# Optimization experiments

Hardware: AMD Instinct MI355X
Metric: run time of the kernel (lower is better)

Reference implementation:

```python
import jax, jax.numpy as jnp
import numpy as np

LAYERS = 2
HEADS = 4
TYPE_IDX = 1  # type='logic' -> 1
HIDDEN = 256
HEAD_DIM = HIDDEN // HEADS
EPS = 1e-6


def setup_inputs() -> dict:
    key = jax.random.key(0)
    ks = jax.random.split(key, 12)
    B, S, H = 4, 2048, HIDDEN
    inputs = jax.random.normal(ks[0], (B, S, H), jnp.float32)
    graphs = jax.random.uniform(ks[1], (B, 2, S, S), jnp.float32)
    biases_batch = jax.random.normal(ks[2], (B, 2, S, S), jnp.float32)
    s_h = 1.0 / np.sqrt(H).astype(np.float32)
    s_d = 1.0 / np.sqrt(HEAD_DIM).astype(np.float32)
    gc_w = jax.random.normal(ks[3], (LAYERS, H, H), jnp.float32) * s_h
    gc_b = jnp.zeros((LAYERS, H), jnp.float32)
    attn_w = jax.random.normal(ks[4], (LAYERS, HEAD_DIM, H), jnp.float32) * s_h  # conv1 (1x1) weight
    attn_a = jax.random.normal(ks[5], (LAYERS, HEAD_DIM), jnp.float32) * s_d     # conv2_1 (1x1) weight
    ln_a = jnp.ones((H,), jnp.float32)
    ln_b = jnp.zeros((H,), jnp.float32)
    w1 = jax.random.normal(ks[6], (H, H), jnp.float32) * s_h
    w1b = jnp.zeros((H,), jnp.float32)
    w2 = jax.random.normal(ks[7], (H, H), jnp.float32) * s_h
    w2b = jnp.zeros((H,), jnp.float32)
    return dict(inputs=inputs, graphs=graphs, biases_batch=biases_batch,
                gc_w=gc_w, gc_b=gc_b, attn_w=attn_w, attn_a=attn_a,
                ln_a=ln_a, ln_b=ln_b, w1=w1, w1b=w1b, w2=w2, w2b=w2b)


def reference(inputs, graphs, biases_batch, gc_w, gc_b, attn_w, attn_a, ln_a, ln_b, w1, w1b, w2, w2b):
    adj = graphs[:, TYPE_IDX]          # [b,s,s]
    bias = biases_batch[:, TYPE_IDX]   # [b,s,s]
    x0 = inputs
    x = inputs
    for i in range(LAYERS):
        # GraphConvolution: adj @ (x @ W) + b
        mf = jnp.einsum('bij,bjh->bih', adj, x @ gc_w[i]) + gc_b[i]
        # Node_Attn_head (NOTE: original uses conv2_1 for BOTH f_1 and f_2)
        seq_fts = jnp.einsum('bsh,dh->bsd', mf, attn_w[i])      # [b,s,d]
        f = seq_fts @ attn_a[i]                                  # [b,s]
        logits = jax.nn.leaky_relu(f[:, :, None] + f[:, None, :])  # f_2^T + f_1 -> [b,s,s]
        coefs = jax.nn.softmax(logits + bias, axis=1)            # Softmax(dim=1)
        ret = jax.nn.leaky_relu(jnp.einsum('bij,bjd->bid', coefs, seq_fts))  # [b,s,d]
        # shared attention head across all HEADS -> identical outputs, concatenated
        x = jnp.tile(ret, (1, 1, HEADS)) + x
    # LayerNorm (torch.std is unbiased -> ddof=1), residual to original inputs
    mean = x.mean(-1, keepdims=True)
    std = jnp.std(x, axis=-1, keepdims=True, ddof=1)
    g = ln_a * (x - mean) / (std + EPS) + ln_b + x0
    # PositionwiseFeedForward (dropout inactive in eval)
    ff = jax.nn.relu(g @ w1.T + w1b) @ w2.T + w2b
    return ff + g
```

## Files before the change

### kernel.cpp

```cpp
#include <hip/hip_runtime.h>
#include <math.h>

#define BB 4
#define SS 2048
#define HH 256
#define DD 64
#define NLAYERS 2
#define NPART 128

#define XSC  (1.f/64.f)
#define XSCI 64.f
#define FSC  (1.f/256.f)
#define WSC  256.f
#define LNWSC 5.5451774444795624f

typedef _Float16 f16;
typedef f16 half8 __attribute__((ext_vector_type(8)));
typedef f16 half4 __attribute__((ext_vector_type(4)));
typedef float f32x4 __attribute__((ext_vector_type(4)));
#define MFMA16(a, b, c) __builtin_amdgcn_mfma_f32_16x16x32_f16(a, b, c, 0, 0, 0)

__device__ __forceinline__ float lrelu(float v) { return v > 0.f ? v : 0.01f * v; }
__device__ __forceinline__ int enc(float f) { int i = __float_as_int(f); return i >= 0 ? i : (i ^ 0x7fffffff); }
__device__ __forceinline__ float dec(int k) { int i = k >= 0 ? k : (k ^ 0x7fffffff); return __int_as_float(i); }
__device__ __forceinline__ void split8(const float* v, half8& h, half8& l) {
    #pragma unroll
    for (int e = 0; e < 8; ++e) {
        f16 hh = (f16)v[e]; h[e] = hh; l[e] = (f16)((v[e] - (float)hh) * 2048.f);
    }
}

__global__ __launch_bounds__(256) void split_scale(
    const float* __restrict__ src, f16* __restrict__ dh, f16* __restrict__ dl, float scale)
{
    long i = ((long)blockIdx.x * 256 + threadIdx.x) * 8;
    float4 a = *(const float4*)&src[i];
    float4 b = *(const float4*)&src[i + 4];
    float v[8] = {a.x * scale, a.y * scale, a.z * scale, a.w * scale,
                  b.x * scale, b.y * scale, b.z * scale, b.w * scale};
    half8 h, l; split8(v, h, l);
    *(half8*)&dh[i] = h; *(half8*)&dl[i] = l;
}

__global__ __launch_bounds__(256) void prep_wy(
    const float* __restrict__ gc_w, const float* __restrict__ gc_b,
    const float* __restrict__ attn_w,
    f16* __restrict__ WysH, f16* __restrict__ WysL, float* __restrict__ by,
    const float* __restrict__ w1, const float* __restrict__ w2,
    f16* __restrict__ w1h, f16* __restrict__ w1l,
    f16* __restrict__ w2h, f16* __restrict__ w2l, int* __restrict__ FMXi)
{
    int L = blockIdx.x >> 6, d = blockIdx.x & 63;
    int h = threadIdx.x;
    const float* gwr = gc_w + (long)L * HH * HH + (long)h * HH;
    const float* aw = attn_w + (long)L * DD * HH + (long)d * HH;
    float acc = 0.f;
    #pragma unroll 4
    for (int hp = 0; hp < HH; hp += 4) {
        float4 g4 = *(const float4*)&gwr[hp];
        float4 a4 = *(const float4*)&aw[hp];
        acc += g4.x * a4.x + g4.y * a4.y + g4.z * a4.z + g4.w * a4.w;
    }
    f16 hh = (f16)acc;
    WysH[((long)L * DD + d) * HH + h] = hh;
    WysL[((long)L * DD + d) * HH + h] = (f16)((acc - (float)hh) * 2048.f);
    if (h == 0) {
        float ba = 0.f;
        const float* gb = gc_b + (long)L * HH;
        for (int hp = 0; hp < HH; ++hp) ba += gb[hp] * aw[hp];
        by[L * DD + d] = ba;
    }
    int gt = blockIdx.x * 256 + h;
    #pragma unroll
    for (int p = 0; p < 4; ++p) {
        int e = gt * 4 + p;
        if (e < 65536) {
            float v = w1[e]; f16 x = (f16)v;
            w1h[e] = x; w1l[e] = (f16)((v - (float)x) * 2048.f);
        } else {
            int e2 = e - 65536;
            float v = w2[e2]; f16 x = (f16)v;
            w2h[e2] = x; w2l[e2] = (f16)((v - (float)x) * 2048.f);
        }
    }
    if (blockIdx.x == 0 && h < 2 * BB) FMXi[h] = enc(-1e30f);
}

__global__ __launch_bounds__(256) void y_mfma(
    const f16* __restrict__ xh, const f16* __restrict__ xl,
    const f16* __restrict__ WyhL, const f16* __restrict__ WylL,
    f16* __restrict__ yTh, f16* __restrict__ yTl)
{
    const int tid = threadIdx.x;
    const int w = tid >> 6, l = tid & 63;
    const int gw = blockIdx.x * 4 + w;
    const int b = gw >> 7, st = gw & 127;
    const int s0 = st * 16;
    const int lr = l & 15, kg = (l >> 4) * 8;
    const f16* Aph = xh + ((long)b * SS + s0 + lr) * HH;
    const f16* Apl = xl + ((long)b * SS + s0 + lr) * HH;
    f32x4 acch[4] = {}, accm[4] = {};
    #pragma unroll
    for (int k0 = 0; k0 < HH; k0 += 32) {
        half8 ah = *(const half8*)(Aph + k0 + kg);
        half8 al = *(const half8*)(Apl + k0 + kg);
        #pragma unroll
        for (int dt = 0; dt < 4; ++dt) {
            long boff = (long)(dt * 16 + lr) * HH + k0 + kg;
            half8 bh = *(const half8*)(WyhL + boff);
            half8 bl = *(const half8*)(WylL + boff);
            acch[dt] = MFMA16(ah, bh, acch[dt]);
            accm[dt] = MFMA16(ah, bl, accm[dt]);
            accm[dt] = MFMA16(al, bh, accm[dt]);
        }
    }
    const int rg0 = (l >> 4) * 4;
    #pragma unroll
    for (int dt = 0; dt < 4; ++dt) {
        int d = dt * 16 + lr;
        half4 h4, l4;
        #pragma unroll
        for (int rr = 0; rr < 4; ++rr) {
            float v = acch[dt][rr] + accm[dt][rr] * (1.f / 2048.f);
            f16 hh = (f16)v; h4[rr] = hh; l4[rr] = (f16)((v - (float)hh) * 2048.f);
        }
        long ob = ((long)b * DD + d) * SS + s0 + rg0;
        *(half4*)(yTh + ob) = h4;
        *(half4*)(yTl + ob) = l4;
    }
}

__global__ __launch_bounds__(512, 2) void ftp_fused(
    const float* __restrict__ adjB,
    const f16* __restrict__ yTh, const f16* __restrict__ yTl,
    const float* __restrict__ byL, const float* __restrict__ aaL,
    float* __restrict__ F, f16* __restrict__ fTh, f16* __restrict__ fTl,
    int* __restrict__ fmxSlot)
{
    __shared__ float Ls[8][16][68];
    __shared__ float fmaxS[16];
    const int b = blockIdx.y;
    const int i0 = blockIdx.x * 16;
    const int tid = threadIdx.x;
    const int w = tid >> 6, l = tid & 63, lr = l & 15, kg = (l >> 4) * 8;
    const float* Arow = adjB + (long)b * 2 * SS * SS + (long)(i0 + lr) * SS;
    const f16* Bh = yTh + ((long)b * DD + lr) * SS;
    const f16* Bl = yTl + ((long)b * DD + lr) * SS;

    f32x4 acch[4] = {}, accm[4] = {};
    #pragma unroll
    for (int ks = 0; ks < 256; ks += 32) {
        int k = w * 256 + ks + kg;
        float4 a0 = *(const float4*)(Arow + k);
        float4 a1 = *(const float4*)(Arow + k + 4);
        float av[8] = {a0.x, a0.y, a0.z, a0.w, a1.x, a1.y, a1.z, a1.w};
        half8 ah, al; split8(av, ah, al);
        #pragma unroll
        for (int dt = 0; dt < 4; ++dt) {
            long off = (long)dt * 16 * SS + k;
            half8 bh = *(const half8*)(Bh + off);
            half8 bl = *(const half8*)(Bl + off);
            acch[dt] = MFMA16(ah, bh, acch[dt]);
            accm[dt] = MFMA16(ah, bl, accm[dt]);
            accm[dt] = MFMA16(al, bh, accm[dt]);
        }
    }
    const int rg0 = (l >> 4) * 4;
    #pragma unroll
    for (int dt = 0; dt < 4; ++dt)
        #pragma unroll
        for (int rr = 0; rr < 4; ++rr)
            Ls[w][rg0 + rr][dt * 16 + lr] = acch[dt][rr] + accm[dt][rr] * (1.f / 2048.f);
    __syncthreads();

    {
        int r = tid >> 5, q = tid & 31, c0 = q * 2;
        float s0 = 0.f, s1 = 0.f;
        #pragma unroll
        for (int ww = 0; ww < 8; ++ww) { s0 += Ls[ww][r][c0]; s1 += Ls[ww][r][c0 + 1]; }
        s0 = s0 * XSCI + byL[c0];
        s1 = s1 * XSCI + byL[c0 + 1];
        Ls[0][r][c0] = s0; Ls[0][r][c0 + 1] = s1;
        float dot = s0 * aaL[c0] + s1 * aaL[c0 + 1];
        dot += __shfl_xor(dot, 1, 64);
        dot += __shfl_xor(dot, 2, 64);
        dot += __shfl_xor(dot, 4, 64);
        dot += __shfl_xor(dot, 8, 64);
        dot += __shfl_xor(dot, 16, 64);
        if (q == 0) { F[b * SS + i0 + r] = dot; fmaxS[r] = dot; }
    }
    __syncthreads();
    if (tid == 0) {
        float m = -1e30f;
        #pragma unroll
        for (int r = 0; r < 16; ++r) m = fmaxf(m, fmaxS[r]);
        atomicMax(fmxSlot + b, enc(m));
    }
    if (tid < 256) {
        int d = tid >> 2, sq = (tid & 3) * 4;
        half4 h4, l4;
        #pragma unroll
        for (int e = 0; e < 4; ++e) {
            float v = Ls[0][sq + e][d] * FSC;
            f16 hh = (f16)v; h4[e] = hh; l4[e] = (f16)((v - (float)hh) * 2048.f);
        }
        long ob = ((long)b * DD + d) * SS + i0 + sq;
        *(half4*)(fTh + ob) = h4;
        *(half4*)(fTl + ob) = l4;
    }
}

__global__ __launch_bounds__(512) void col_stats_part(
    const float* __restrict__ biasb, const float* __restrict__ f,
    const int* __restrict__ fmxSlot,
    float* __restrict__ partS, float* __restrict__ Mv)
{
    __shared__ float fs[32];
    const int b = blockIdx.z;
    const int chunk = blockIdx.y;
    const int half = threadIdx.x >> 8;
    const int t = threadIdx.x & 255;
    const int j0 = blockIdx.x * 1024 + t * 4;
    const float* bb = biasb + (long)b * 2 * SS * SS;
    const int ibase = chunk * 32 + half * 16;

    if (threadIdx.x < 32) fs[threadIdx.x] = f[b * SS + chunk * 32 + threadIdx.x];

    float fj[4], M[4], s[4] = {0.f, 0.f, 0.f, 0.f};
    const float fmx = dec(fmxSlot[b]);
    #pragma unroll
    for (int q = 0; q < 4; ++q) {
        fj[q] = f[b * SS + j0 + q];
        M[q] = lrelu(fmx + fj[q]) + 8.f;
    }
    __syncthreads();

    #pragma unroll
    for (int ii = 0; ii < 16; ii += 2) {
        float fi0 = fs[half * 16 + ii], fi1 = fs[half * 16 + ii + 1];
        float4 b0 = *(const float4*)&bb[(long)(ibase + ii) * SS + j0];
        float4 b1 = *(const float4*)&bb[(long)(ibase + ii + 1) * SS + j0];
        s[0] += __expf(lrelu(fi0 + fj[0]) + b0.x - M[0]);
        s[1] += __expf(lrelu(fi0 + fj[1]) + b0.y - M[1]);
        s[2] += __expf(lrelu(fi0 + fj[2]) + b0.z - M[2]);
        s[3] += __expf(lrelu(fi0 + fj[3]) + b0.w - M[3]);
        s[0] += __expf(lrelu(fi1 + fj[0]) + b1.x - M[0]);
        s[1] += __expf(lrelu(fi1 + fj[1]) + b1.y - M[1]);
        s[2] += __expf(lrelu(fi1 + fj[2]) + b1.z - M[2]);
        s[3] += __expf(lrelu(fi1 + fj[3]) + b1.w - M[3]);
    }
    const int c = chunk * 2 + half;
    #pragma unroll
    for (int q = 0; q < 4; ++q)
        partS[((long)c * BB + b) * SS + j0 + q] = s[q];
    if (chunk == 0 && half == 0) {
        #pragma unroll
        for (int q = 0; q < 4; ++q) Mv[b * SS + j0 + q] = M[q];
    }
}

__global__ __launch_bounds__(256) void col_stats_merge(
    const float* __restrict__ partS, const float* __restrict__ Mv,
    float* __restrict__ Cv)
{
    __shared__ float red[4][64];
    const int b = blockIdx.y;
    const int jl = threadIdx.x & 63;
    const int p = threadIdx.x >> 6;
    const int j = blockIdx.x * 64 + jl;
    float s = 0.f;
    #pragma unroll
    for (int k = 0; k < 32; ++k)
        s += partS[((long)(p * 32 + k) * BB + b) * SS + j];
    red[p][jl] = s;
    __syncthreads();
    if (p == 0) {
        float tot = ((red[0][jl] + red[1][jl]) + (red[2][jl] + red[3][jl]));
        Cv[b * SS + j] = LNWSC - __logf(tot) - Mv[b * SS + j];
    }
}

__global__ __launch_bounds__(512, 2) void pvp_fused(
    const float* __restrict__ biasb, const float* __restrict__ f,
    const float* __restrict__ Cv,
    const f16* __restrict__ fTh, const f16* __restrict__ fTl,
    const float* __restrict__ xin, float* __restrict__ X,
    f16* __restrict__ xh, f16* __restrict__ xl, int writeSplit)
{
    __shared__ float Ls[8][16][68];
    const int b = blockIdx.y;
    const int i0 = blockIdx.x * 16;
    const int tid = threadIdx.x;
    const int w = tid >> 6, l = tid & 63, lr = l & 15, kg = (l >> 4) * 8;
    const int irow = i0 + lr;
    const float fi = f[b * SS + irow];
    const float* brow = biasb + (long)b * 2 * SS * SS + (long)irow * SS;
    const float* fb = f + b * SS;
    const float* cb = Cv + b * SS;
    const f16* Bh = fTh + ((long)b * DD + lr) * SS;
    const f16* Bl = fTl + ((long)b * DD + lr) * SS;

    f32x4 acch[4] = {}, accm[4] = {};
    #pragma unroll
    for (int jc = 0; jc < 256; jc += 32) {
        const int jb = w * 256 + jc + kg;
        float4 bs0 = *(const float4*)(brow + jb);
        float4 bs1 = *(const float4*)(brow + jb + 4);
        float4 fj0 = *(const float4*)(fb + jb);
        float4 fj1 = *(const float4*)(fb + jb + 4);
        float4 cj0 = *(const float4*)(cb + jb);
        float4 cj1 = *(const float4*)(cb + jb + 4);
        float wv[8];
        wv[0] = __expf(lrelu(fi + fj0.x) + bs0.x + cj0.x);
        wv[1] = __expf(lrelu(fi + fj0.y) + bs0.y + cj0.y);
        wv[2] = __expf(lrelu(fi + fj0.z) + bs0.z + cj0.z);
        wv[3] = __expf(lrelu(fi + fj0.w) + bs0.w + cj0.w);
        wv[4] = __expf(lrelu(fi + fj1.x) + bs1.x + cj1.x);
        wv[5] = __expf(lrelu(fi + fj1.y) + bs1.y + cj1.y);
        wv[6] = __expf(lrelu(fi + fj1.z) + bs1.z + cj1.z);
        wv[7] = __expf(lrelu(fi + fj1.w) + bs1.w + cj1.w);
        half8 ah, al; split8(wv, ah, al);
        #pragma unroll
        for (int dt = 0; dt < 4; ++dt) {
            long off = (long)dt * 16 * SS + jb;
            half8 bh = *(const half8*)(Bh + off);
            half8 bl = *(const half8*)(Bl + off);
            acch[dt] = MFMA16(ah, bh, acch[dt]);
            accm[dt] = MFMA16(ah, bl, accm[dt]);
            accm[dt] = MFMA16(al, bh, accm[dt]);
        }
    }
    const int rg0 = (l >> 4) * 4;
    #pragma unroll
    for (int dt = 0; dt < 4; ++dt)
        #pragma unroll
        for (int rr = 0; rr < 4; ++rr)
            Ls[w][rg0 + rr][dt * 16 + lr] = acch[dt][rr] + accm[dt][rr] * (1.f / 2048.f);
    __syncthreads();

    {
        int r = tid >> 5, q = tid & 31, dq = q * 2;
        float v0 = 0.f, v1 = 0.f;
        #pragma unroll
        for (int ww = 0; ww < 8; ++ww) { v0 += Ls[ww][r][dq]; v1 += Ls[ww][r][dq + 1]; }
        v0 = lrelu(v0); v1 = lrelu(v1);
        long rowoff = ((long)b * SS + i0 + r) * HH;
        #pragma unroll
        for (int rep = 0; rep < 4; ++rep) {
            long off = rowoff + rep * DD + dq;
            float o0 = v0 + xin[off];
            float o1 = v1 + xin[off + 1];
            X[off] = o0; X[off + 1] = o1;
            if (writeSplit) {
                float s0 = o0 * XSC, s1 = o1 * XSC;
                f16 h0 = (f16)s0, h1 = (f16)s1;
                xh[off] = h0; xl[off] = (f16)((s0 - (float)h0) * 2048.f);
                xh[off + 1] = h1; xl[off + 1] = (f16)((s1 - (float)h1) * 2048.f);
            }
        }
    }
}

__global__ __launch_bounds__(256) void layernorm_g(
    const float* __restrict__ x, const float* __restrict__ x0,
    const float* __restrict__ lna, const float* __restrict__ lnb,
    float* __restrict__ g, f16* __restrict__ gh, f16* __restrict__ gl)
{
    const int wave = threadIdx.x >> 6, lane = threadIdx.x & 63;
    const long row = (long)blockIdx.x * 4 + wave;
    const int c0 = lane * 4;
    float4 v = *(const float4*)&x[row * HH + c0];
    float s = v.x + v.y + v.z + v.w;
    #pragma unroll
    for (int off = 32; off; off >>= 1) s += __shfl_xor(s, off, 64);
    float mean = s * (1.f / HH);
    float dx = v.x - mean, dy = v.y - mean, dz = v.z - mean, dw = v.w - mean;
    float sq = dx * dx + dy * dy + dz * dz + dw * dw;
    #pragma unroll
    for (int off = 32; off; off >>= 1) sq += __shfl_xor(sq, off, 64);
    float stdv = sqrtf(sq * (1.f / (HH - 1)));
    float rinv = 1.f / (stdv + 1e-6f);
    float4 la = *(const float4*)&lna[c0];
    float4 lb = *(const float4*)&lnb[c0];
    float4 xo = *(const float4*)&x0[row * HH + c0];
    float gv[4];
    gv[0] = la.x * dx * rinv + lb.x + xo.x;
    gv[1] = la.y * dy * rinv + lb.y + xo.y;
    gv[2] = la.z * dz * rinv + lb.z + xo.z;
    gv[3] = la.w * dw * rinv + lb.w + xo.w;
    *(float4*)&g[row * HH + c0] = *(float4*)gv;
    half4 h4, l4;
    #pragma unroll
    for (int e = 0; e < 4; ++e) {
        f16 hh = (f16)gv[e]; h4[e] = hh; l4[e] = (f16)((gv[e] - (float)hh) * 2048.f);
    }
    *(half4*)&gh[row * HH + c0] = h4;
    *(half4*)&gl[row * HH + c0] = l4;
}

__global__ __launch_bounds__(256) void ffn_mfma(
    const f16* __restrict__ Ah, const f16* __restrict__ Al,
    const f16* __restrict__ Bh, const f16* __restrict__ Bl,
    const float* __restrict__ bias, const float* __restrict__ res,
    float* __restrict__ outF, f16* __restrict__ outH, f16* __restrict__ outL,
    int doRelu)
{
    __shared__ float Ls[64][68];
    const int i0 = blockIdx.x * 64, j0 = blockIdx.y * 64;
    const int tid = threadIdx.x;
    const int w = tid >> 6, l = tid & 63, lr = l & 15, kg = (l >> 4) * 8;
    const f16* Aph = Ah + ((long)i0 + w * 16 + lr) * HH;
    const f16* Apl = Al + ((long)i0 + w * 16 + lr) * HH;
    f32x4 acch[4] = {}, accm[4] = {};
    #pragma unroll
    for (int k0 = 0; k0 < HH; k0 += 32) {
        half8 ah = *(const half8*)(Aph + k0 + kg);
        half8 al = *(const half8*)(Apl + k0 + kg);
        #pragma unroll
        for (int dt = 0; dt < 4; ++dt) {
            long boff = ((long)(j0 + dt * 16 + lr)) * HH + k0 + kg;
            half8 bh = *(const half8*)(Bh + boff);
            half8 bl = *(const half8*)(Bl + boff);
            acch[dt] = MFMA16(ah, bh, acch[dt]);
            accm[dt] = MFMA16(ah, bl, accm[dt]);
            accm[dt] = MFMA16(al, bh, accm[dt]);
        }
    }
    const int rg0 = (l >> 4) * 4;
    #pragma unroll
    for (int dt = 0; dt < 4; ++dt) {
        float bj = bias[j0 + dt * 16 + lr];
        #pragma unroll
        for (int rr = 0; rr < 4; ++rr) {
            float v = acch[dt][rr] + accm[dt][rr] * (1.f / 2048.f) + bj;
            if (doRelu) v = fmaxf(v, 0.f);
            Ls[w * 16 + rg0 + rr][dt * 16 + lr] = v;
        }
    }
    __syncthreads();
    int s = tid >> 2, nq = (tid & 3) * 16;
    long go = ((long)i0 + s) * HH + j0 + nq;
    if (outF) {
        #pragma unroll
        for (int q = 0; q < 4; ++q) {
            float4 v = *(float4*)&Ls[s][nq + q * 4];
            if (res) {
                float4 r = *(const float4*)&res[go + q * 4];
                v.x += r.x; v.y += r.y; v.z += r.z; v.w += r.w;
            }
            *(float4*)&outF[go + q * 4] = v;
        }
    } else {
        float v0[8], v1[8];
        #pragma unroll
        for (int e = 0; e < 8; ++e) { v0[e] = Ls[s][nq + e]; v1[e] = Ls[s][nq + 8 + e]; }
        half8 h0, l0, h1, l1; split8(v0, h0, l0); split8(v1, h1, l1);
        *(half8*)&outH[go] = h0; *(half8*)&outH[go + 8] = h1;
        *(half8*)&outL[go] = l0; *(half8*)&outL[go + 8] = l1;
    }
}

extern "C" void kernel_launch(void* const* d_in, const int* in_sizes, int n_in,
                              void* d_out, int out_size, void* d_ws, size_t ws_size,
                              hipStream_t stream)
{
    const float* inputs = (const float*)d_in[0];
    const float* graphs = (const float*)d_in[1];
    const float* biases = (const float*)d_in[2];
    const float* gc_w   = (const float*)d_in[3];
    const float* gc_b   = (const float*)d_in[4];
    const float* attn_w = (const float*)d_in[5];
    const float* attn_a = (const float*)d_in[6];
    const float* ln_a   = (const float*)d_in[7];
    const float* ln_b   = (const float*)d_in[8];
    const float* w1     = (const float*)d_in[9];
    const float* w1b    = (const float*)d_in[10];
    const float* w2     = (const float*)d_in[11];
    const float* w2b    = (const float*)d_in[12];
    float* out = (float*)d_out;

    float* ws   = (float*)d_ws;
    float* X    = ws;
    float* G    = ws + 2097152;
    float* PTS  = ws + 4194304;
    float* F    = ws + 5242880;
    float* Mv   = ws + 5251072;
    float* Cv   = ws + 5259264;
    float* by   = ws + 5267456;
    int*   FMXi = (int*)(ws + 5267584);
    f16* WysH   = (f16*)(ws + 5267712);
    f16* WysL   = (f16*)(ws + 5284096);
    f16* yTh    = (f16*)(ws + 5300480);
    f16* yTl    = (f16*)(ws + 5562624);
    f16* fTh    = (f16*)(ws + 5824768);
    f16* fTl    = (f16*)(ws + 6086912);
    f16* xh     = (f16*)(ws + 6349056);
    f16* xl     = (f16*)(ws + 7397632);
    f16* gh     = (f16*)(ws + 8446208);
    f16* gl     = (f16*)(ws + 9494784);
    f16* h1h    = (f16*)(ws + 10543360);
    f16* h1l    = (f16*)(ws + 11591936);
    f16* w1h    = (f16*)(ws + 12640512);
    f16* w1l    = (f16*)(ws + 12673280);
    f16* w2h    = (f16*)(ws + 12706048);
    f16* w2l    = (f16*)(ws + 12738816);

    const float* adjBase  = graphs + (long)SS * SS;
    const float* biasBase = biases + (long)SS * SS;

    prep_wy<<<128, 256, 0, stream>>>(gc_w, gc_b, attn_w, WysH, WysL, by,
                                     w1, w2, w1h, w1l, w2h, w2l, FMXi);
    split_scale<<<1024, 256, 0, stream>>>(inputs, xh, xl, XSC);

    for (int L = 0; L < NLAYERS; ++L) {
        y_mfma<<<128, 256, 0, stream>>>(xh, xl,
            WysH + (long)L * DD * HH, WysL + (long)L * DD * HH, yTh, yTl);
        ftp_fused<<<dim3(128, BB), 512, 0, stream>>>(
            adjBase, yTh, yTl, by + L * DD, attn_a + (long)L * DD,
            F, fTh, fTl, FMXi + L * BB);
        col_stats_part<<<dim3(2, 64, BB), 512, 0, stream>>>(
            biasBase, F, FMXi + L * BB, PTS, Mv);
        col_stats_merge<<<dim3(32, BB), 256, 0, stream>>>(PTS, Mv, Cv);
        pvp_fused<<<dim3(128, BB), 512, 0, stream>>>(
            biasBase, F, Cv, fTh, fTl,
            (L == 0) ? inputs : X, X, xh, xl, (L == 0) ? 1 : 0);
    }

    layernorm_g<<<2048, 256, 0, stream>>>(X, inputs, ln_a, ln_b, G, gh, gl);
    ffn_mfma<<<dim3(128, 4), 256, 0, stream>>>(gh, gl, w1h, w1l, w1b,
                                               nullptr, nullptr, h1h, h1l, 1);
    ffn_mfma<<<dim3(128, 4), 256, 0, stream>>>(h1h, h1l, w2h, w2l, w2b,
                                               G, out, nullptr, nullptr, 0);
}
```

Measured before the change: 303.8 us.

## Merge prep kernels, prefetch A/bias loads, double col-stat partitions, pack f and C

Folds the input split/scale kernel into the weight prep kernel to save a launch. Adds software prefetch of the next adjacency and bias tiles in ftp_fused and pvp_fused, so global loads overlap the MFMA work. Doubles the number of column-stat partitions (half the rows per block, twice the blocks) for more parallelism, at the cost of a longer merge loop. Packs f and the column normaliser into one float2 array so pvp reads one stream instead of two, and moves workspace offsets to fit the larger partial buffer.

```diff
diff --git a/kernel.cpp b/kernel.cpp
--- a/kernel.cpp
+++ b/kernel.cpp
@@ -6,7 +6,7 @@
 #define HH 256
 #define DD 64
 #define NLAYERS 2
-#define NPART 128
+#define NPART 256
 
 #define XSC  (1.f/64.f)
 #define XSCI 64.f
@@ -30,26 +30,25 @@
     }
 }
 
-__global__ __launch_bounds__(256) void split_scale(
-    const float* __restrict__ src, f16* __restrict__ dh, f16* __restrict__ dl, float scale)
-{
-    long i = ((long)blockIdx.x * 256 + threadIdx.x) * 8;
-    float4 a = *(const float4*)&src[i];
-    float4 b = *(const float4*)&src[i + 4];
-    float v[8] = {a.x * scale, a.y * scale, a.z * scale, a.w * scale,
-                  b.x * scale, b.y * scale, b.z * scale, b.w * scale};
-    half8 h, l; split8(v, h, l);
-    *(half8*)&dh[i] = h; *(half8*)&dl[i] = l;
-}
-
-__global__ __launch_bounds__(256) void prep_wy(
+__global__ __launch_bounds__(256) void prep_all(
     const float* __restrict__ gc_w, const float* __restrict__ gc_b,
     const float* __restrict__ attn_w,
     f16* __restrict__ WysH, f16* __restrict__ WysL, float* __restrict__ by,
     const float* __restrict__ w1, const float* __restrict__ w2,
     f16* __restrict__ w1h, f16* __restrict__ w1l,
-    f16* __restrict__ w2h, f16* __restrict__ w2l, int* __restrict__ FMXi)
-{
+    f16* __restrict__ w2h, f16* __restrict__ w2l, int* __restrict__ FMXi,
+    const float* __restrict__ inputs, f16* __restrict__ xh, f16* __restrict__ xl)
+{
+    if (blockIdx.x >= 128) {
+        long i = ((long)(blockIdx.x - 128) * 256 + threadIdx.x) * 8;
+        float4 a = *(const float4*)&inputs[i];
+        float4 b = *(const float4*)&inputs[i + 4];
+        float v[8] = {a.x * XSC, a.y * XSC, a.z * XSC, a.w * XSC,
+                      b.x * XSC, b.y * XSC, b.z * XSC, b.w * XSC};
+        half8 h, l; split8(v, h, l);
+        *(half8*)&xh[i] = h; *(half8*)&xl[i] = l;
+        return;
+    }
     int L = blockIdx.x >> 6, d = blockIdx.x & 63;
     int h = threadIdx.x;
     const float* gwr = gc_w + (long)L * HH * HH + (long)h * HH;
@@ -148,12 +147,18 @@
     const f16* Bl = yTl + ((long)b * DD + lr) * SS;
 
     f32x4 acch[4] = {}, accm[4] = {};
+    float4 a0 = *(const float4*)(Arow + w * 256 + kg);
+    float4 a1 = *(const float4*)(Arow + w * 256 + kg + 4);
     #pragma unroll
     for (int ks = 0; ks < 256; ks += 32) {
+        float4 c0 = a0, c1 = a1;
+        if (ks < 224) {
+            int nk = w * 256 + ks + 32 + kg;
+            a0 = *(const float4*)(Arow + nk);
+            a1 = *(const float4*)(Arow + nk + 4);
+        }
         int k = w * 256 + ks + kg;
-        float4 a0 = *(const float4*)(Arow + k);
-        float4 a1 = *(const float4*)(Arow + k + 4);
-        float av[8] = {a0.x, a0.y, a0.z, a0.w, a1.x, a1.y, a1.z, a1.w};
+        float av[8] = {c0.x, c0.y, c0.z, c0.w, c1.x, c1.y, c1.z, c1.w};
         half8 ah, al; split8(av, ah, al);
         #pragma unroll
         for (int dt = 0; dt < 4; ++dt) {
@@ -215,16 +220,16 @@
     const int* __restrict__ fmxSlot,
     float* __restrict__ partS, float* __restrict__ Mv)
 {
-    __shared__ float fs[32];
+    __shared__ float fs[16];
     const int b = blockIdx.z;
     const int chunk = blockIdx.y;
     const int half = threadIdx.x >> 8;
     const int t = threadIdx.x & 255;
     const int j0 = blockIdx.x * 1024 + t * 4;
     const float* bb = biasb + (long)b * 2 * SS * SS;
-    const int ibase = chunk * 32 + half * 16;
-
-    if (threadIdx.x < 32) fs[threadIdx.x] = f[b * SS + chunk * 32 + threadIdx.x];
+    const int ibase = chunk * 16 + half * 8;
+
+    if (threadIdx.x < 16) fs[threadIdx.x] = f[b * SS + chunk * 16 + threadIdx.x];
 
     float fj[4], M[4], s[4] = {0.f, 0.f, 0.f, 0.f};
     const float fmx = dec(fmxSlot[b]);
@@ -236,8 +241,8 @@
     __syncthreads();
 
     #pragma unroll
-    for (int ii = 0; ii < 16; ii += 2) {
-        float fi0 = fs[half * 16 + ii], fi1 = fs[half * 16 + ii + 1];
+    for (int ii = 0; ii < 8; ii += 2) {
+        float fi0 = fs[half * 8 + ii], fi1 = fs[half * 8 + ii + 1];
         float4 b0 = *(const float4*)&bb[(long)(ibase + ii) * SS + j0];
         float4 b1 = *(const float4*)&bb[(long)(ibase + ii + 1) * SS + j0];
         s[0] += __expf(lrelu(fi0 + fj[0]) + b0.x - M[0]);
@@ -253,7 +258,7 @@
     #pragma unroll
     for (int q = 0; q < 4; ++q)
         partS[((long)c * BB + b) * SS + j0 + q] = s[q];
-    if (chunk == 0 && half == 0) {
+    if (c == 0) {
         #pragma unroll
         for (int q = 0; q < 4; ++q) Mv[b * SS + j0 + q] = M[q];
     }
@@ -261,7 +266,7 @@
 
 __global__ __launch_bounds__(256) void col_stats_merge(
     const float* __restrict__ partS, const float* __restrict__ Mv,
-    float* __restrict__ Cv)
+    const float* __restrict__ f, float2* __restrict__ FC)
 {
     __shared__ float red[4][64];
     const int b = blockIdx.y;
@@ -270,19 +275,22 @@
     const int j = blockIdx.x * 64 + jl;
     float s = 0.f;
     #pragma unroll
-    for (int k = 0; k < 32; ++k)
-        s += partS[((long)(p * 32 + k) * BB + b) * SS + j];
+    for (int k = 0; k < 64; ++k)
+        s += partS[((long)(p * 64 + k) * BB + b) * SS + j];
     red[p][jl] = s;
     __syncthreads();
     if (p == 0) {
         float tot = ((red[0][jl] + red[1][jl]) + (red[2][jl] + red[3][jl]));
-        Cv[b * SS + j] = LNWSC - __logf(tot) - Mv[b * SS + j];
+        float2 fc;
+        fc.x = f[b * SS + j];
+        fc.y = LNWSC - __logf(tot) - Mv[b * SS + j];
+        FC[b * SS + j] = fc;
     }
 }
 
 __global__ __launch_bounds__(512, 2) void pvp_fused(
     const float* __restrict__ biasb, const float* __restrict__ f,
-    const float* __restrict__ Cv,
+    const float2* __restrict__ FC,
     const f16* __restrict__ fTh, const f16* __restrict__ fTl,
     const float* __restrict__ xin, float* __restrict__ X,
     f16* __restrict__ xh, f16* __restrict__ xl, int writeSplit)
@@ -295,30 +303,35 @@
     const int irow = i0 + lr;
     const float fi = f[b * SS + irow];
     const float* brow = biasb + (long)b * 2 * SS * SS + (long)irow * SS;
-    const float* fb = f + b * SS;
-    const float* cb = Cv + b * SS;
+    const float2* fcb = FC + (long)b * SS;
     const f16* Bh = fTh + ((long)b * DD + lr) * SS;
     const f16* Bl = fTl + ((long)b * DD + lr) * SS;
 
     f32x4 acch[4] = {}, accm[4] = {};
+    float4 pb0 = *(const float4*)(brow + w * 256 + kg);
+    float4 pb1 = *(const float4*)(brow + w * 256 + kg + 4);
     #pragma unroll
     for (int jc = 0; jc < 256; jc += 32) {
+        float4 bs0 = pb0, bs1 = pb1;
+        if (jc < 224) {
+            int nj = w * 256 + jc + 32 + kg;
+            pb0 = *(const float4*)(brow + nj);
+            pb1 = *(const float4*)(brow + nj + 4);
+        }
         const int jb = w * 256 + jc + kg;
-        float4 bs0 = *(const float4*)(brow + jb);
-        float4 bs1 = *(const float4*)(brow + jb + 4);
-        float4 fj0 = *(const float4*)(fb + jb);
-        float4 fj1 = *(const float4*)(fb + jb + 4);
-        float4 cj0 = *(const float4*)(cb + jb);
-        float4 cj1 = *(const float4*)(cb + jb + 4);
+        float4 fc0 = *(const float4*)&fcb[jb];
+        float4 fc1 = *(const float4*)&fcb[jb + 2];
+        float4 fc2 = *(const float4*)&fcb[jb + 4];
+        float4 fc3 = *(const float4*)&fcb[jb + 6];
         float wv[8];
-        wv[0] = __expf(lrelu(fi + fj0.x) + bs0.x + cj0.x);
-        wv[1] = __expf(lrelu(fi + fj0.y) + bs0.y + cj0.y);
-        wv[2] = __expf(lrelu(fi + fj0.z) + bs0.z + cj0.z);
-        wv[3] = __expf(lrelu(fi + fj0.w) + bs0.w + cj0.w);
-        wv[4] = __expf(lrelu(fi + fj1.x) + bs1.x + cj1.x);
-        wv[5] = __expf(lrelu(fi + fj1.y) + bs1.y + cj1.y);
-        wv[6] = __expf(lrelu(fi + fj1.z) + bs1.z + cj1.z);
-        wv[7] = __expf(lrelu(fi + fj1.w) + bs1.w + cj1.w);
+        wv[0] = __expf(lrelu(fi + fc0.x) + bs0.x + fc0.y);
+        wv[1] = __expf(lrelu(fi + fc0.z) + bs0.y + fc0.w);
+        wv[2] = __expf(lrelu(fi + fc1.x) + bs0.z + fc1.y);
+        wv[3] = __expf(lrelu(fi + fc1.z) + bs0.w + fc1.w);
+        wv[4] = __expf(lrelu(fi + fc2.x) + bs1.x + fc2.y);
+        wv[5] = __expf(lrelu(fi + fc2.z) + bs1.y + fc2.w);
+        wv[6] = __expf(lrelu(fi + fc3.x) + bs1.z + fc3.y);
+        wv[7] = __expf(lrelu(fi + fc3.z) + bs1.w + fc3.w);
         half8 ah, al; split8(wv, ah, al);
         #pragma unroll
         for (int dt = 0; dt < 4; ++dt) {
@@ -483,34 +496,34 @@
     float* X    = ws;
     float* G    = ws + 2097152;
     float* PTS  = ws + 4194304;
-    float* F    = ws + 5242880;
-    float* Mv   = ws + 5251072;
-    float* Cv   = ws + 5259264;
-    float* by   = ws + 5267456;
-    int*   FMXi = (int*)(ws + 5267584);
-    f16* WysH   = (f16*)(ws + 5267712);
-    f16* WysL   = (f16*)(ws + 5284096);
-    f16* yTh    = (f16*)(ws + 5300480);
-    f16* yTl    = (f16*)(ws + 5562624);
-    f16* fTh    = (f16*)(ws + 5824768);
-    f16* fTl    = (f16*)(ws + 6086912);
-    f16* xh     = (f16*)(ws + 6349056);
-    f16* xl     = (f16*)(ws + 7397632);
-    f16* gh     = (f16*)(ws + 8446208);
-    f16* gl     = (f16*)(ws + 9494784);
-    f16* h1h    = (f16*)(ws + 10543360);
-    f16* h1l    = (f16*)(ws + 11591936);
-    f16* w1h    = (f16*)(ws + 12640512);
-    f16* w1l    = (f16*)(ws + 12673280);
-    f16* w2h    = (f16*)(ws + 12706048);
-    f16* w2l    = (f16*)(ws + 12738816);
+    float* F    = ws + 6291456;
+    float* Mv   = ws + 6299648;
+    float2* FC  = (float2*)(ws + 6307840);
+    float* by   = ws + 6324224;
+    int*   FMXi = (int*)(ws + 6324352);
+    f16* WysH   = (f16*)(ws + 6324480);
+    f16* WysL   = (f16*)(ws + 6340864);
+    f16* yTh    = (f16*)(ws + 6357248);
+    f16* yTl    = (f16*)(ws + 6619392);
+    f16* fTh    = (f16*)(ws + 6881536);
+    f16* fTl    = (f16*)(ws + 7143680);
+    f16* xh     = (f16*)(ws + 7405824);
+    f16* xl     = (f16*)(ws + 8454400);
+    f16* gh     = (f16*)(ws + 9502976);
+    f16* gl     = (f16*)(ws + 10551552);
+    f16* h1h    = (f16*)(ws + 11600128);
+    f16* h1l    = (f16*)(ws + 12648704);
+    f16* w1h    = (f16*)(ws + 13697280);
+    f16* w1l    = (f16*)(ws + 13730048);
+    f16* w2h    = (f16*)(ws + 13762816);
+    f16* w2l    = (f16*)(ws + 13795584);
 
     const float* adjBase  = graphs + (long)SS * SS;
     const float* biasBase = biases + (long)SS * SS;
 
-    prep_wy<<<128, 256, 0, stream>>>(gc_w, gc_b, attn_w, WysH, WysL, by,
-                                     w1, w2, w1h, w1l, w2h, w2l, FMXi);
-    split_scale<<<1024, 256, 0, stream>>>(inputs, xh, xl, XSC);
+    prep_all<<<1152, 256, 0, stream>>>(gc_w, gc_b, attn_w, WysH, WysL, by,
+                                       w1, w2, w1h, w1l, w2h, w2l, FMXi,
+                                       inputs, xh, xl);
 
     for (int L = 0; L < NLAYERS; ++L) {
         y_mfma<<<128, 256, 0, stream>>>(xh, xl,
@@ -518,11 +531,11 @@
         ftp_fused<<<dim3(128, BB), 512, 0, stream>>>(
             adjBase, yTh, yTl, by + L * DD, attn_a + (long)L * DD,
             F, fTh, fTl, FMXi + L * BB);
-        col_stats_part<<<dim3(2, 64, BB), 512, 0, stream>>>(
+        col_stats_part<<<dim3(2, 128, BB), 512, 0, stream>>>(
             biasBase, F, FMXi + L * BB, PTS, Mv);
-        col_stats_merge<<<dim3(32, BB), 256, 0, stream>>>(PTS, Mv, Cv);
+        col_stats_merge<<<dim3(32, BB), 256, 0, stream>>>(PTS, Mv, F, FC);
         pvp_fused<<<dim3(128, BB), 512, 0, stream>>>(
-            biasBase, F, Cv, fTh, fTl,
+            biasBase, F, FC, fTh, fTl,
             (L == 0) ? inputs : X, X, xh, xl, (L == 0) ? 1 : 0);
     }
 
```

After: 337.1 us. +10.9%, slower.
